# Optimization experiments

Hardware: AMD Instinct MI355X
Metric: run time of the kernel (lower is better)

The kernel has to match this reference:

```python
import jax, jax.numpy as jnp
from jax import lax
import numpy as np

B, S = 128, 512
TARGET_SIZE = 32
T = TARGET_SIZE + 4  # tag_size, START = T-2, END = T-1


def setup_inputs() -> dict:
    key = jax.random.key(0)
    k1, k2, k3, k4 = jax.random.split(key, 4)
    feats = jax.random.normal(k1, (B, S, T), dtype=jnp.float32)
    # contiguous-prefix mask (lengths in [S//2, S])
    lengths = jax.random.randint(k2, (B,), S // 2, S + 1)
    mask = (jnp.arange(S)[None, :] < lengths[:, None]).astype(jnp.int32)
    tags = jax.random.randint(k3, (B, S), 0, TARGET_SIZE).astype(jnp.int32)
    # learned transitions, with the hard constraints from __init__
    transitions = 0.1 * jax.random.normal(k4, (T, T), dtype=jnp.float32)
    transitions = transitions.at[:, T - 2].set(-1000.0)  # nothing -> START
    transitions = transitions.at[T - 1, :].set(-1000.0)  # END -> nothing
    return {"feats": feats, "transitions": transitions, "mask": mask, "tags": tags}


def _nll(feats, transitions, mask, tags):
    # feats: (B,S,T), transitions: (T,T) with [i,j] = score(prev=i -> cur=j)
    b, s, t = feats.shape
    START, END = t - 2, t - 1
    fdtype = feats.dtype

    feats_t = jnp.swapaxes(feats, 0, 1)   # (S,B,T)
    mask_t = jnp.swapaxes(mask, 0, 1)     # (S,B)

    # ---- forward algorithm (partition function) ----
    # scores[t,b,i,j] = feats[b,t,j] + transitions[i,j]
    part0 = feats_t[0] + transitions[START][None, :]  # (B,T): alpha after step 0

    def step(part, xs):
        f_step, m_step = xs  # (B,T), (B,)
        # cur[b,i,j] = feats[b,j] + trans[i,j] + part[b,i]
        cur = f_step[:, None, :] + transitions[None, :, :] + part[:, :, None]
        new_part = jax.nn.logsumexp(cur, axis=1)  # (B,T)
        part = jnp.where(m_step[:, None].astype(bool), new_part, part)
        return part, None

    part, _ = lax.scan(step, part0, (feats_t[1:], mask_t[1:]))
    final = jax.nn.logsumexp(part[:, :, None] + transitions[None, :, :], axis=1)  # (B,T)
    forward_score = jnp.sum(final[:, END])

    # ---- gold score ----
    tags_i = tags.astype(jnp.int32)
    prev_tags = jnp.concatenate(
        [jnp.full((b, 1), START, dtype=jnp.int32), tags_i[:, :-1]], axis=1)  # (B,S)
    emit = jnp.take_along_axis(feats, tags_i[:, :, None], axis=2)[:, :, 0]    # (B,S)
    trans_sc = transitions[prev_tags, tags_i]                                  # (B,S)
    tg_energy = jnp.sum((emit + trans_sc) * mask.astype(fdtype))
    lengths = jnp.sum(mask, axis=1).astype(jnp.int32)                          # (B,)
    end_ids = jnp.take_along_axis(tags_i, (lengths - 1)[:, None], axis=1)[:, 0]
    end_energy = jnp.sum(transitions[end_ids, END])
    gold_score = tg_energy + end_energy

    # average_batch = True
    return (forward_score - gold_score) / jnp.asarray(b, fdtype)


def reference(feats, transitions, mask, tags):
    return _nll(feats, transitions, mask, tags)
```

## Files before the change

### kernel.cpp

```cpp
#include <hip/hip_runtime.h>
#include <hip/hip_bf16.h>


namespace {
constexpr int kB = 128;
constexpr int kS = 512;
constexpr int kT = 36;
constexpr int kStart = 34;
constexpr int kEnd = 35;
constexpr int kP = 32;
constexpr int kL = 16;
constexpr int kEStr = 64;

typedef __bf16 bf16x4 __attribute__((ext_vector_type(4)));
typedef short short4v __attribute__((ext_vector_type(4)));
typedef float f32x4 __attribute__((ext_vector_type(4)));
typedef int int2v __attribute__((ext_vector_type(2)));

__device__ __forceinline__ float readlane_f(float v, int lane) {
    return __builtin_bit_cast(float, __builtin_amdgcn_readlane(__builtin_bit_cast(int, v), lane));
}

__device__ __forceinline__ float wave_sum(float v) {
#pragma unroll
    for (int off = 32; off; off >>= 1) v += __shfl_xor(v, off, 64);
    return v;
}

__device__ __forceinline__ int wave_sum_i(int v) {
#pragma unroll
    for (int off = 32; off; off >>= 1) v += __shfl_xor(v, off, 64);
    return v;
}

#define MF16(a, b, c) __builtin_amdgcn_mfma_f32_16x16x16bf16_1k((a), (b), (c), 0, 0, 0)


__global__ __attribute__((amdgpu_flat_work_group_size(64, 64),
                          amdgpu_waves_per_eu(2, 4)))
void crf_chunk_kernel(const float* __restrict__ feats,
                      const float* __restrict__ trans,
                      const int* __restrict__ mask,
                      __bf16* __restrict__ Hws,
                      float* __restrict__ lscws) {
    const int b = blockIdx.x;
    const int p = blockIdx.y;
    const int tid = threadIdx.x;
    const int ln = tid & 15;
    const int quad = tid >> 4;

    __shared__ __align__(16) float Etab[kL * kEStr];

    const int* mb = mask + b * kS;
    int len = 0;
#pragma unroll
    for (int k = 0; k < kS / 64; ++k) len += mb[k * 64 + tid];
    len = wave_sum_i(len);

    __bf16* Hout = Hws + (size_t)(b * kP + p) * (kT * kT);
    const int cs = (p == 0) ? 1 : p * kL;
    const int ce = min((p + 1) * kL, len);
    const int nsteps = ce - cs;

    if (nsteps <= 0) {
        for (int idx = tid; idx < kT * kT; idx += 64)
            Hout[idx] = (__bf16)((idx / kT == idx % kT) ? 1.f : 0.f);
        if (tid == 0) lscws[b * kP + p] = 0.f;
        return;
    }

    const float* fb = feats + ((size_t)b * kS + cs) * kT;
    {
        float stage[kL];
#pragma unroll
        for (int it = 0; it < kL; ++it)
            stage[it] = (tid < kT) ? fb[it * kT + tid] : 0.f;
#pragma unroll
        for (int it = 0; it < kL; ++it)
            Etab[it * kEStr + tid] = (tid < kT) ? __expf(stage[it]) : 1.0f;
    }
    __builtin_amdgcn_s_waitcnt(0);

    auto afrag = [&](int rt, int kc) {
        bf16x4 r;
        const int m = rt * 16 + ln;
#pragma unroll
        for (int e = 0; e < 4; ++e) {
            const int k = kc * 16 + quad * 4 + e;
            float v = 0.f;
            if (m < kT && k < kT) v = __expf(trans[k * kT + m]);
            r[e] = (__bf16)v;
        }
        return __builtin_bit_cast(short4v, r);
    };
    const short4v a00 = afrag(0, 0), a01 = afrag(0, 1), a02 = afrag(0, 2);
    const short4v a10 = afrag(1, 0), a11 = afrag(1, 1), a12 = afrag(1, 2);
    const short4v a20 = afrag(2, 0), a21 = afrag(2, 1), a22 = afrag(2, 2);

    auto binit = [&](int kc, int ct) {
        bf16x4 r;
        const int n = ct * 16 + ln;
#pragma unroll
        for (int e = 0; e < 4; ++e) {
            const int k = kc * 16 + quad * 4 + e;
            r[e] = (__bf16)((k == n && k < kT) ? 1.f : 0.f);
        }
        return __builtin_bit_cast(short4v, r);
    };
    short4v b00 = binit(0, 0), b01 = binit(0, 1), b02 = binit(0, 2);
    short4v b10 = binit(1, 0), b11 = binit(1, 1), b12 = binit(1, 2);
    short4v b20 = binit(2, 0), b21 = binit(2, 1), b22 = binit(2, 2);

    float logC = 0.f;
    const f32x4 z = {0.f, 0.f, 0.f, 0.f};
    for (int tl = 0; tl < nsteps; ++tl) {
        const int w11 = __builtin_amdgcn_readlane(__builtin_bit_cast(int2v, b00).x, 1);
        const float* et = &Etab[tl * kEStr + quad * 4];
        const f32x4 e0 = *(const f32x4*)(et + 0);
        const f32x4 e1 = *(const f32x4*)(et + 16);
        const f32x4 e2 = *(const f32x4*)(et + 32);

        f32x4 c00 = MF16(a00, b00, z); f32x4 c01 = MF16(a00, b01, z); f32x4 c02 = MF16(a00, b02, z);
        c00 = MF16(a01, b10, c00);     c01 = MF16(a01, b11, c01);     c02 = MF16(a01, b12, c02);
        c00 = MF16(a02, b20, c00);     c01 = MF16(a02, b21, c01);     c02 = MF16(a02, b22, c02);
        f32x4 c10 = MF16(a10, b00, z); f32x4 c11 = MF16(a10, b01, z); f32x4 c12 = MF16(a10, b02, z);
        c10 = MF16(a11, b10, c10);     c11 = MF16(a11, b11, c11);     c12 = MF16(a11, b12, c12);
        c10 = MF16(a12, b20, c10);     c11 = MF16(a12, b21, c11);     c12 = MF16(a12, b22, c12);
        f32x4 c20 = MF16(a20, b00, z); f32x4 c21 = MF16(a20, b01, z); f32x4 c22 = MF16(a20, b02, z);
        c20 = MF16(a21, b10, c20);     c21 = MF16(a21, b11, c21);     c22 = MF16(a21, b12, c22);
        c20 = MF16(a22, b20, c20);     c21 = MF16(a22, b21, c21);     c22 = MF16(a22, b22, c22);

        float rs = 1.f;
        if ((tl & 3) == 3) {
            const float s = __builtin_bit_cast(float, (unsigned)w11 & 0xFFFF0000u);
            rs = __builtin_amdgcn_rcpf(s);
            logC += __logf(s);
        }
        const f32x4 s0 = e0 * rs, s1 = e1 * rs, s2 = e2 * rs;

#define PK(cv, sv) ({ const f32x4 t_ = (cv) * (sv); bf16x4 h_;                  \
        h_[0] = (__bf16)t_[0]; h_[1] = (__bf16)t_[1];                           \
        h_[2] = (__bf16)t_[2]; h_[3] = (__bf16)t_[3];                           \
        __builtin_bit_cast(short4v, h_); })
        b00 = PK(c00, s0); b01 = PK(c01, s0); b02 = PK(c02, s0);
        b10 = PK(c10, s1); b11 = PK(c11, s1); b12 = PK(c12, s1);
        b20 = PK(c20, s2); b21 = PK(c21, s2); b22 = PK(c22, s2);
#undef PK
    }

#define STOREB(Bv, kc, ct) {                                                    \
    const bf16x4 h_ = __builtin_bit_cast(bf16x4, Bv);                           \
    const int n_ = (ct)*16 + ln;                                                \
    _Pragma("unroll") for (int e = 0; e < 4; ++e) {                             \
        const int m_ = (kc)*16 + quad * 4 + e;                                  \
        if (m_ < kT && n_ < kT) Hout[m_ * kT + n_] = h_[e]; } }
    STOREB(b00, 0, 0) STOREB(b01, 0, 1) STOREB(b02, 0, 2)
    STOREB(b10, 1, 0) STOREB(b11, 1, 1) STOREB(b12, 1, 2)
    STOREB(b20, 2, 0) STOREB(b21, 2, 1) STOREB(b22, 2, 2)
#undef STOREB
    if (tid == 0) lscws[b * kP + p] = logC;
}


#define FORK36(X) \
    X(0,0,0,0) X(1,1,0,1) X(2,2,0,2) X(3,3,0,3) \
    X(4,0,1,0) X(5,1,1,1) X(6,2,1,2) X(7,3,1,3) \
    X(8,0,2,0) X(9,1,2,1) X(10,2,2,2) X(11,3,2,3) \
    X(12,0,3,0) X(13,1,3,1) X(14,2,3,2) X(15,3,3,3) \
    X(16,0,4,0) X(17,1,4,1) X(18,2,4,2) X(19,3,4,3) \
    X(20,0,5,0) X(21,1,5,1) X(22,2,5,2) X(23,3,5,3) \
    X(24,0,6,0) X(25,1,6,1) X(26,2,6,2) X(27,3,6,3) \
    X(28,0,7,0) X(29,1,7,1) X(30,2,7,2) X(31,3,7,3) \
    X(32,0,8,0) X(33,1,8,1) X(34,2,8,2) X(35,3,8,3)

__global__ __attribute__((amdgpu_flat_work_group_size(64, 64),
                          amdgpu_waves_per_eu(1, 1)))
void crf_combine_kernel(const float* __restrict__ feats,
                        const float* __restrict__ trans,
                        const int* __restrict__ mask,
                        const int* __restrict__ tags,
                        const __bf16* __restrict__ Hws,
                        const float* __restrict__ lscws,
                        float* __restrict__ out) {
    const int b = blockIdx.x;
    const int j = threadIdx.x;
    const float* fbase = feats + (size_t)b * kS * kT;
    const int* mb = mask + b * kS;
    const int* tb = tags + b * kS;

    int len = 0;
#pragma unroll
    for (int k = 0; k < kS / 64; ++k) len += mb[k * 64 + j];
    len = wave_sum_i(len);

    const float ME = (j < kT) ? __expf(trans[j * kT + kEnd]) : 0.f;

    float a0 = -1e30f;
    if (j < kT) a0 = fbase[j] + trans[kStart * kT + j];
    float C = readlane_f(a0, 0);
    float q = __expf(a0 - C);

    const int jr = (j < kT) ? j : 0;
#pragma unroll 4
    for (int p = 0; p < kP; ++p) {
        const __bf16* rp = Hws + ((size_t)(b * kP + p) * kT + jr) * kT;
        const bf16x4 h0 = *(const bf16x4*)(rp + 0);
        const bf16x4 h1 = *(const bf16x4*)(rp + 4);
        const bf16x4 h2 = *(const bf16x4*)(rp + 8);
        const bf16x4 h3 = *(const bf16x4*)(rp + 12);
        const bf16x4 h4 = *(const bf16x4*)(rp + 16);
        const bf16x4 h5 = *(const bf16x4*)(rp + 20);
        const bf16x4 h6 = *(const bf16x4*)(rp + 24);
        const bf16x4 h7 = *(const bf16x4*)(rp + 28);
        const bf16x4 h8 = *(const bf16x4*)(rp + 32);
#define BRD2(n, a, g, c) const float bb##n = readlane_f(q, n);
        FORK36(BRD2)
#undef BRD2
        float v0 = 0.f, v1 = 0.f, v2 = 0.f, v3 = 0.f;
#define FMA2(n, a, g, c) v##a = fmaf(bb##n, (float)h##g[c], v##a);
        FORK36(FMA2)
#undef FMA2
        const float qn = (v0 + v1) + (v2 + v3);
        q = (j < kT) ? qn : 0.f;
        C += lscws[b * kP + p];
        const float s = readlane_f(q, 0);
        q *= __builtin_amdgcn_rcpf(s);
        C += __logf(s);
    }

    const float ssum = wave_sum(q * ME);
    const float forward_b = C + __logf(ssum);

    float g = 0.f;
    for (int k = j; k < kS; k += 64) {
        if (k < len) {
            const int tg = tb[k];
            const int pv = (k == 0) ? kStart : tb[k - 1];
            g += fbase[(size_t)k * kT + tg] + trans[pv * kT + tg];
        }
    }
    g = wave_sum(g);

    if (j == 0) {
        g += trans[tb[len - 1] * kT + kEnd];
        atomicAdd(out, (forward_b - g) * (1.0f / kB));
    }
}

}

extern "C" void kernel_launch(void* const* d_in, const int* in_sizes, int n_in,
                              void* d_out, int out_size, void* d_ws, size_t ws_size,
                              hipStream_t stream) {
    const float* feats = (const float*)d_in[0];
    const float* trans = (const float*)d_in[1];
    const int* mask = (const int*)d_in[2];
    const int* tags = (const int*)d_in[3];
    float* out = (float*)d_out;

    __bf16* Hws = (__bf16*)d_ws;
    float* lscws = (float*)(Hws + (size_t)kB * kP * kT * kT);

    (void)hipMemsetAsync(out, 0, sizeof(float), stream);
    crf_chunk_kernel<<<dim3(kB, kP), dim3(64), 0, stream>>>(feats, trans, mask, Hws, lscws);
    crf_combine_kernel<<<dim3(kB), dim3(64), 0, stream>>>(feats, trans, mask, tags,
                                                          Hws, lscws, out);
}
```

Baseline: 109.6 us.

## Add tree-merge stage of chunk transfer matrices and pack four chunks per block

Adds an intermediate merge kernel that multiplies groups of eight chunk transfer matrices together with MFMA, so the final serial combine walks four matrices per sequence instead of thirty-two. The chunk kernel now runs four waves per block, each handling one chunk with its own shared-memory exp table. This shortens the serial dependency chain in the final kernel at the cost of an extra kernel launch, an extra workspace round trip, and more bf16 rounding from the additional matrix products.

```diff
diff --git a/kernel.cpp b/kernel.cpp
--- a/kernel.cpp
+++ b/kernel.cpp
@@ -10,7 +10,8 @@
 constexpr int kEnd = 35;
 constexpr int kP = 32;
 constexpr int kL = 16;
-constexpr int kEStr = 64;
+constexpr int kG = 4;
+constexpr int kEStr = 48;
 
 typedef __bf16 bf16x4 __attribute__((ext_vector_type(4)));
 typedef short short4v __attribute__((ext_vector_type(4)));
@@ -35,37 +36,54 @@
 
 #define MF16(a, b, c) __builtin_amdgcn_mfma_f32_16x16x16bf16_1k((a), (b), (c), 0, 0, 0)
 
-
-__global__ __attribute__((amdgpu_flat_work_group_size(64, 64),
-                          amdgpu_waves_per_eu(2, 4)))
+#define MM27()                                                                               \
+    f32x4 c00 = MF16(a00, b00, z); f32x4 c01 = MF16(a00, b01, z); f32x4 c02 = MF16(a00, b02, z); \
+    c00 = MF16(a01, b10, c00);     c01 = MF16(a01, b11, c01);     c02 = MF16(a01, b12, c02);     \
+    c00 = MF16(a02, b20, c00);     c01 = MF16(a02, b21, c01);     c02 = MF16(a02, b22, c02);     \
+    f32x4 c10 = MF16(a10, b00, z); f32x4 c11 = MF16(a10, b01, z); f32x4 c12 = MF16(a10, b02, z); \
+    c10 = MF16(a11, b10, c10);     c11 = MF16(a11, b11, c11);     c12 = MF16(a11, b12, c12);     \
+    c10 = MF16(a12, b20, c10);     c11 = MF16(a12, b21, c11);     c12 = MF16(a12, b22, c12);     \
+    f32x4 c20 = MF16(a20, b00, z); f32x4 c21 = MF16(a20, b01, z); f32x4 c22 = MF16(a20, b02, z); \
+    c20 = MF16(a21, b10, c20);     c21 = MF16(a21, b11, c21);     c22 = MF16(a21, b12, c22);     \
+    c20 = MF16(a22, b20, c20);     c21 = MF16(a22, b21, c21);     c22 = MF16(a22, b22, c22);
+
+#define PK(cv, sv) ({ const f32x4 t_ = (cv) * (sv); bf16x4 h_;                  \
+        h_[0] = (__bf16)t_[0]; h_[1] = (__bf16)t_[1];                           \
+        h_[2] = (__bf16)t_[2]; h_[3] = (__bf16)t_[3];                           \
+        __builtin_bit_cast(short4v, h_); })
+
+
+__global__ __attribute__((amdgpu_flat_work_group_size(256, 256),
+                          amdgpu_waves_per_eu(4, 8)))
 void crf_chunk_kernel(const float* __restrict__ feats,
                       const float* __restrict__ trans,
                       const int* __restrict__ mask,
-                      __bf16* __restrict__ Hws,
-                      float* __restrict__ lscws) {
+                      __bf16* __restrict__ Hc,
+                      float* __restrict__ lsc) {
     const int b = blockIdx.x;
-    const int p = blockIdx.y;
-    const int tid = threadIdx.x;
-    const int ln = tid & 15;
-    const int quad = tid >> 4;
-
-    __shared__ __align__(16) float Etab[kL * kEStr];
+    const int wid = threadIdx.x >> 6;
+    const int lane = threadIdx.x & 63;
+    const int p = blockIdx.y * 4 + wid;
+    const int ln = lane & 15;
+    const int quad = lane >> 4;
+
+    __shared__ __align__(16) float Etab[4][kL * kEStr];
 
     const int* mb = mask + b * kS;
     int len = 0;
 #pragma unroll
-    for (int k = 0; k < kS / 64; ++k) len += mb[k * 64 + tid];
+    for (int k = 0; k < kS / 64; ++k) len += mb[k * 64 + lane];
     len = wave_sum_i(len);
 
-    __bf16* Hout = Hws + (size_t)(b * kP + p) * (kT * kT);
+    __bf16* Hout = Hc + (size_t)(b * kP + p) * (kT * kT);
     const int cs = (p == 0) ? 1 : p * kL;
     const int ce = min((p + 1) * kL, len);
     const int nsteps = ce - cs;
 
     if (nsteps <= 0) {
-        for (int idx = tid; idx < kT * kT; idx += 64)
+        for (int idx = lane; idx < kT * kT; idx += 64)
             Hout[idx] = (__bf16)((idx / kT == idx % kT) ? 1.f : 0.f);
-        if (tid == 0) lscws[b * kP + p] = 0.f;
+        if (lane == 0) lsc[b * kP + p] = 0.f;
         return;
     }
 
@@ -74,10 +92,11 @@
         float stage[kL];
 #pragma unroll
         for (int it = 0; it < kL; ++it)
-            stage[it] = (tid < kT) ? fb[it * kT + tid] : 0.f;
+            stage[it] = (lane < kT) ? fb[it * kT + lane] : 0.f;
 #pragma unroll
         for (int it = 0; it < kL; ++it)
-            Etab[it * kEStr + tid] = (tid < kT) ? __expf(stage[it]) : 1.0f;
+            if (lane < kEStr)
+                Etab[wid][it * kEStr + lane] = (lane < kT) ? __expf(stage[it]) : 1.0f;
     }
     __builtin_amdgcn_s_waitcnt(0);
 
@@ -115,20 +134,12 @@
     const f32x4 z = {0.f, 0.f, 0.f, 0.f};
     for (int tl = 0; tl < nsteps; ++tl) {
         const int w11 = __builtin_amdgcn_readlane(__builtin_bit_cast(int2v, b00).x, 1);
-        const float* et = &Etab[tl * kEStr + quad * 4];
+        const float* et = &Etab[wid][tl * kEStr + quad * 4];
         const f32x4 e0 = *(const f32x4*)(et + 0);
         const f32x4 e1 = *(const f32x4*)(et + 16);
         const f32x4 e2 = *(const f32x4*)(et + 32);
 
-        f32x4 c00 = MF16(a00, b00, z); f32x4 c01 = MF16(a00, b01, z); f32x4 c02 = MF16(a00, b02, z);
-        c00 = MF16(a01, b10, c00);     c01 = MF16(a01, b11, c01);     c02 = MF16(a01, b12, c02);
-        c00 = MF16(a02, b20, c00);     c01 = MF16(a02, b21, c01);     c02 = MF16(a02, b22, c02);
-        f32x4 c10 = MF16(a10, b00, z); f32x4 c11 = MF16(a10, b01, z); f32x4 c12 = MF16(a10, b02, z);
-        c10 = MF16(a11, b10, c10);     c11 = MF16(a11, b11, c11);     c12 = MF16(a11, b12, c12);
-        c10 = MF16(a12, b20, c10);     c11 = MF16(a12, b21, c11);     c12 = MF16(a12, b22, c12);
-        f32x4 c20 = MF16(a20, b00, z); f32x4 c21 = MF16(a20, b01, z); f32x4 c22 = MF16(a20, b02, z);
-        c20 = MF16(a21, b10, c20);     c21 = MF16(a21, b11, c21);     c22 = MF16(a21, b12, c22);
-        c20 = MF16(a22, b20, c20);     c21 = MF16(a22, b21, c21);     c22 = MF16(a22, b22, c22);
+        MM27()
 
         float rs = 1.f;
         if ((tl & 3) == 3) {
@@ -137,15 +148,9 @@
             logC += __logf(s);
         }
         const f32x4 s0 = e0 * rs, s1 = e1 * rs, s2 = e2 * rs;
-
-#define PK(cv, sv) ({ const f32x4 t_ = (cv) * (sv); bf16x4 h_;                  \
-        h_[0] = (__bf16)t_[0]; h_[1] = (__bf16)t_[1];                           \
-        h_[2] = (__bf16)t_[2]; h_[3] = (__bf16)t_[3];                           \
-        __builtin_bit_cast(short4v, h_); })
         b00 = PK(c00, s0); b01 = PK(c01, s0); b02 = PK(c02, s0);
         b10 = PK(c10, s1); b11 = PK(c11, s1); b12 = PK(c12, s1);
         b20 = PK(c20, s2); b21 = PK(c21, s2); b22 = PK(c22, s2);
-#undef PK
     }
 
 #define STOREB(Bv, kc, ct) {                                                    \
@@ -157,8 +162,88 @@
     STOREB(b00, 0, 0) STOREB(b01, 0, 1) STOREB(b02, 0, 2)
     STOREB(b10, 1, 0) STOREB(b11, 1, 1) STOREB(b12, 1, 2)
     STOREB(b20, 2, 0) STOREB(b21, 2, 1) STOREB(b22, 2, 2)
-#undef STOREB
-    if (tid == 0) lscws[b * kP + p] = logC;
+    if (lane == 0) lsc[b * kP + p] = logC;
+}
+
+
+__global__ __attribute__((amdgpu_flat_work_group_size(64, 64),
+                          amdgpu_waves_per_eu(1, 4)))
+void crf_merge_kernel(const __bf16* __restrict__ Hc,
+                      const float* __restrict__ lsc,
+                      __bf16* __restrict__ Hm,
+                      float* __restrict__ mlsc) {
+    const int b = blockIdx.x;
+    const int g = blockIdx.y;
+    const int lane = threadIdx.x;
+    const int ln = lane & 15;
+    const int quad = lane >> 4;
+    const int base = b * kP + g * 8;
+
+    float logm = 0.f;
+#pragma unroll
+    for (int i = 0; i < 8; ++i) logm += lsc[base + i];
+
+    const __bf16* H0 = Hc + (size_t)base * (kT * kT);
+    auto loadB0 = [&](int kc, int ct) {
+        bf16x4 r;
+        const int n = ct * 16 + ln;
+#pragma unroll
+        for (int e = 0; e < 4; ++e) {
+            const int k = kc * 16 + quad * 4 + e;
+            float v = 0.f;
+            if (k < kT && n < kT) v = (float)H0[k * kT + n];
+            r[e] = (__bf16)v;
+        }
+        return __builtin_bit_cast(short4v, r);
+    };
+    short4v b00 = loadB0(0, 0), b01 = loadB0(0, 1), b02 = loadB0(0, 2);
+    short4v b10 = loadB0(1, 0), b11 = loadB0(1, 1), b12 = loadB0(1, 2);
+    short4v b20 = loadB0(2, 0), b21 = loadB0(2, 1), b22 = loadB0(2, 2);
+
+    const f32x4 z = {0.f, 0.f, 0.f, 0.f};
+    for (int i = 1; i < 8; ++i) {
+        const __bf16* Hn = Hc + (size_t)(base + i) * (kT * kT);
+        auto loadA = [&](int rt, int kc) {
+            bf16x4 r;
+            const int m = rt * 16 + ln;
+            const int k0 = kc * 16 + quad * 4;
+            if (m < kT && k0 + 3 < kT) {
+                r = *(const bf16x4*)&Hn[m * kT + k0];
+            } else {
+#pragma unroll
+                for (int e = 0; e < 4; ++e)
+                    r[e] = (__bf16)((m < kT && k0 + e < kT) ? (float)Hn[m * kT + k0 + e] : 0.f);
+            }
+            return __builtin_bit_cast(short4v, r);
+        };
+        const short4v a00 = loadA(0, 0), a01 = loadA(0, 1), a02 = loadA(0, 2);
+        const short4v a10 = loadA(1, 0), a11 = loadA(1, 1), a12 = loadA(1, 2);
+        const short4v a20 = loadA(2, 0), a21 = loadA(2, 1), a22 = loadA(2, 2);
+
+        const int w11 = __builtin_amdgcn_readlane(__builtin_bit_cast(int2v, b00).x, 1);
+
+        MM27()
+
+        const float s = __builtin_bit_cast(float, (unsigned)w11 & 0xFFFF0000u);
+        const float rsf = __builtin_amdgcn_rcpf(s);
+        logm += __logf(s);
+        const f32x4 rv = {rsf, rsf, rsf, rsf};
+        b00 = PK(c00, rv); b01 = PK(c01, rv); b02 = PK(c02, rv);
+        b10 = PK(c10, rv); b11 = PK(c11, rv); b12 = PK(c12, rv);
+        b20 = PK(c20, rv); b21 = PK(c21, rv); b22 = PK(c22, rv);
+    }
+
+    __bf16* Ho = Hm + (size_t)(b * kG + g) * (kT * kT);
+#define STOREM(Bv, kc, ct) {                                                    \
+    const bf16x4 h_ = __builtin_bit_cast(bf16x4, Bv);                           \
+    const int n_ = (ct)*16 + ln;                                                \
+    _Pragma("unroll") for (int e = 0; e < 4; ++e) {                             \
+        const int m_ = (kc)*16 + quad * 4 + e;                                  \
+        if (m_ < kT && n_ < kT) Ho[m_ * kT + n_] = h_[e]; } }
+    STOREM(b00, 0, 0) STOREM(b01, 0, 1) STOREM(b02, 0, 2)
+    STOREM(b10, 1, 0) STOREM(b11, 1, 1) STOREM(b12, 1, 2)
+    STOREM(b20, 2, 0) STOREM(b21, 2, 1) STOREM(b22, 2, 2)
+    if (lane == 0) mlsc[b * kG + g] = logm;
 }
 
 
@@ -175,13 +260,13 @@
 
 __global__ __attribute__((amdgpu_flat_work_group_size(64, 64),
                           amdgpu_waves_per_eu(1, 1)))
-void crf_combine_kernel(const float* __restrict__ feats,
-                        const float* __restrict__ trans,
-                        const int* __restrict__ mask,
-                        const int* __restrict__ tags,
-                        const __bf16* __restrict__ Hws,
-                        const float* __restrict__ lscws,
-                        float* __restrict__ out) {
+void crf_final_kernel(const float* __restrict__ feats,
+                      const float* __restrict__ trans,
+                      const int* __restrict__ mask,
+                      const int* __restrict__ tags,
+                      const __bf16* __restrict__ Hm,
+                      const float* __restrict__ mlsc,
+                      float* __restrict__ out) {
     const int b = blockIdx.x;
     const int j = threadIdx.x;
     const float* fbase = feats + (size_t)b * kS * kT;
@@ -201,9 +286,9 @@
     float q = __expf(a0 - C);
 
     const int jr = (j < kT) ? j : 0;
-#pragma unroll 4
-    for (int p = 0; p < kP; ++p) {
-        const __bf16* rp = Hws + ((size_t)(b * kP + p) * kT + jr) * kT;
+#pragma unroll
+    for (int g = 0; g < kG; ++g) {
+        const __bf16* rp = Hm + ((size_t)(b * kG + g) * kT + jr) * kT;
         const bf16x4 h0 = *(const bf16x4*)(rp + 0);
         const bf16x4 h1 = *(const bf16x4*)(rp + 4);
         const bf16x4 h2 = *(const bf16x4*)(rp + 8);
@@ -213,16 +298,16 @@
         const bf16x4 h6 = *(const bf16x4*)(rp + 24);
         const bf16x4 h7 = *(const bf16x4*)(rp + 28);
         const bf16x4 h8 = *(const bf16x4*)(rp + 32);
-#define BRD2(n, a, g, c) const float bb##n = readlane_f(q, n);
+#define BRD2(n, a, g2, c) const float bb##n = readlane_f(q, n);
         FORK36(BRD2)
 #undef BRD2
         float v0 = 0.f, v1 = 0.f, v2 = 0.f, v3 = 0.f;
-#define FMA2(n, a, g, c) v##a = fmaf(bb##n, (float)h##g[c], v##a);
+#define FMA2(n, a, g2, c) v##a = fmaf(bb##n, (float)h##g2[c], v##a);
         FORK36(FMA2)
 #undef FMA2
         const float qn = (v0 + v1) + (v2 + v3);
         q = (j < kT) ? qn : 0.f;
-        C += lscws[b * kP + p];
+        C += mlsc[b * kG + g];
         const float s = readlane_f(q, 0);
         q *= __builtin_amdgcn_rcpf(s);
         C += __logf(s);
@@ -231,19 +316,19 @@
     const float ssum = wave_sum(q * ME);
     const float forward_b = C + __logf(ssum);
 
-    float g = 0.f;
+    float g2 = 0.f;
     for (int k = j; k < kS; k += 64) {
         if (k < len) {
             const int tg = tb[k];
             const int pv = (k == 0) ? kStart : tb[k - 1];
-            g += fbase[(size_t)k * kT + tg] + trans[pv * kT + tg];
-        }
-    }
-    g = wave_sum(g);
+            g2 += fbase[(size_t)k * kT + tg] + trans[pv * kT + tg];
+        }
+    }
+    g2 = wave_sum(g2);
 
     if (j == 0) {
-        g += trans[tb[len - 1] * kT + kEnd];
-        atomicAdd(out, (forward_b - g) * (1.0f / kB));
+        g2 += trans[tb[len - 1] * kT + kEnd];
+        atomicAdd(out, (forward_b - g2) * (1.0f / kB));
     }
 }
 
@@ -258,11 +343,14 @@
     const int* tags = (const int*)d_in[3];
     float* out = (float*)d_out;
 
-    __bf16* Hws = (__bf16*)d_ws;
-    float* lscws = (float*)(Hws + (size_t)kB * kP * kT * kT);
+    __bf16* Hc = (__bf16*)d_ws;
+    float* lsc = (float*)(Hc + (size_t)kB * kP * kT * kT);
+    __bf16* Hm = (__bf16*)(lsc + kB * kP);
+    float* mlsc = (float*)(Hm + (size_t)kB * kG * kT * kT);
 
     (void)hipMemsetAsync(out, 0, sizeof(float), stream);
-    crf_chunk_kernel<<<dim3(kB, kP), dim3(64), 0, stream>>>(feats, trans, mask, Hws, lscws);
-    crf_combine_kernel<<<dim3(kB), dim3(64), 0, stream>>>(feats, trans, mask, tags,
-                                                          Hws, lscws, out);
-}
+    crf_chunk_kernel<<<dim3(kB, kP / 4), dim3(256), 0, stream>>>(feats, trans, mask, Hc, lsc);
+    crf_merge_kernel<<<dim3(kB, kG), dim3(64), 0, stream>>>(Hc, lsc, Hm, mlsc);
+    crf_final_kernel<<<dim3(kB), dim3(64), 0, stream>>>(feats, trans, mask, tags,
+                                                        Hm, mlsc, out);
+}
```

Result: no change. 110.3 us (+0.7%).

## Process two chunks per block with interleaved MFMA chains and pre-multiply pairs

Applied to the files above, without the earlier changes.

Each chunk block now computes two adjacent 16-step transfer-matrix products at once, interleaving their independent MFMA chains to hide MFMA latency. It then multiplies the two products together in-block through an LDS transpose. This halves the number of matrices the serial combine kernel must fold per batch (16 instead of 32) and halves the grid size. The cost is higher register pressure, an extra 36x36 matmul per block, and fewer blocks for occupancy.

```diff
diff --git a/kernel.cpp b/kernel.cpp
--- a/kernel.cpp
+++ b/kernel.cpp
@@ -8,9 +8,10 @@
 constexpr int kT = 36;
 constexpr int kStart = 34;
 constexpr int kEnd = 35;
-constexpr int kP = 32;
 constexpr int kL = 16;
-constexpr int kEStr = 64;
+constexpr int kG = 16;
+constexpr int kEStr = 48;
+constexpr int kTS = 52;
 
 typedef __bf16 bf16x4 __attribute__((ext_vector_type(4)));
 typedef short short4v __attribute__((ext_vector_type(4)));
@@ -35,49 +36,72 @@
 
 #define MF16(a, b, c) __builtin_amdgcn_mfma_f32_16x16x16bf16_1k((a), (b), (c), 0, 0, 0)
 
+#define MM27(AP, BP, CP) \
+    f32x4 CP##_00 = MF16(AP##_00, BP##_00, z), CP##_01 = MF16(AP##_00, BP##_01, z), CP##_02 = MF16(AP##_00, BP##_02, z); \
+    f32x4 CP##_10 = MF16(AP##_10, BP##_00, z), CP##_11 = MF16(AP##_10, BP##_01, z), CP##_12 = MF16(AP##_10, BP##_02, z); \
+    f32x4 CP##_20 = MF16(AP##_20, BP##_00, z), CP##_21 = MF16(AP##_20, BP##_01, z), CP##_22 = MF16(AP##_20, BP##_02, z); \
+    CP##_00 = MF16(AP##_01, BP##_10, CP##_00); CP##_01 = MF16(AP##_01, BP##_11, CP##_01); CP##_02 = MF16(AP##_01, BP##_12, CP##_02); \
+    CP##_10 = MF16(AP##_11, BP##_10, CP##_10); CP##_11 = MF16(AP##_11, BP##_11, CP##_11); CP##_12 = MF16(AP##_11, BP##_12, CP##_12); \
+    CP##_20 = MF16(AP##_21, BP##_10, CP##_20); CP##_21 = MF16(AP##_21, BP##_11, CP##_21); CP##_22 = MF16(AP##_21, BP##_12, CP##_22); \
+    CP##_00 = MF16(AP##_02, BP##_20, CP##_00); CP##_01 = MF16(AP##_02, BP##_21, CP##_01); CP##_02 = MF16(AP##_02, BP##_22, CP##_02); \
+    CP##_10 = MF16(AP##_12, BP##_20, CP##_10); CP##_11 = MF16(AP##_12, BP##_21, CP##_11); CP##_12 = MF16(AP##_12, BP##_22, CP##_12); \
+    CP##_20 = MF16(AP##_22, BP##_20, CP##_20); CP##_21 = MF16(AP##_22, BP##_21, CP##_21); CP##_22 = MF16(AP##_22, BP##_22, CP##_22);
+
+#define PK(cv, sv) ({ const f32x4 t_ = (cv) * (sv); bf16x4 h_;                  \
+        h_[0] = (__bf16)t_[0]; h_[1] = (__bf16)t_[1];                           \
+        h_[2] = (__bf16)t_[2]; h_[3] = (__bf16)t_[3];                           \
+        __builtin_bit_cast(short4v, h_); })
+
 
 __global__ __attribute__((amdgpu_flat_work_group_size(64, 64),
                           amdgpu_waves_per_eu(2, 4)))
-void crf_chunk_kernel(const float* __restrict__ feats,
-                      const float* __restrict__ trans,
-                      const int* __restrict__ mask,
-                      __bf16* __restrict__ Hws,
-                      float* __restrict__ lscws) {
+void crf_pair_kernel(const float* __restrict__ feats,
+                     const float* __restrict__ trans,
+                     const int* __restrict__ mask,
+                     __bf16* __restrict__ Hp,
+                     float* __restrict__ lsc) {
     const int b = blockIdx.x;
-    const int p = blockIdx.y;
-    const int tid = threadIdx.x;
-    const int ln = tid & 15;
-    const int quad = tid >> 4;
-
-    __shared__ __align__(16) float Etab[kL * kEStr];
+    const int g = blockIdx.y;
+    const int lane = threadIdx.x;
+    const int ln = lane & 15;
+    const int quad = lane >> 4;
+
+    __shared__ __align__(16) float Etab[2 * kL * kEStr];
+    __shared__ __align__(16) unsigned short Tr[48 * kTS];
 
     const int* mb = mask + b * kS;
     int len = 0;
 #pragma unroll
-    for (int k = 0; k < kS / 64; ++k) len += mb[k * 64 + tid];
+    for (int k = 0; k < kS / 64; ++k) len += mb[k * 64 + lane];
     len = wave_sum_i(len);
 
-    __bf16* Hout = Hws + (size_t)(b * kP + p) * (kT * kT);
-    const int cs = (p == 0) ? 1 : p * kL;
-    const int ce = min((p + 1) * kL, len);
-    const int nsteps = ce - cs;
-
-    if (nsteps <= 0) {
-        for (int idx = tid; idx < kT * kT; idx += 64)
+    __bf16* Hout = Hp + (size_t)(b * kG + g) * (kT * kT);
+    const int p0 = 2 * g, p1 = 2 * g + 1;
+    const int cs0 = (p0 == 0) ? 1 : p0 * kL;
+    const int n0 = min((p0 + 1) * kL, len) - cs0;
+    const int cs1 = p1 * kL;
+    const int n1 = min((p1 + 1) * kL, len) - cs1;
+
+    if (n0 <= 0) {
+        for (int idx = lane; idx < kT * kT; idx += 64)
             Hout[idx] = (__bf16)((idx / kT == idx % kT) ? 1.f : 0.f);
-        if (tid == 0) lscws[b * kP + p] = 0.f;
+        if (lane == 0) lsc[b * kG + g] = 0.f;
         return;
     }
 
-    const float* fb = feats + ((size_t)b * kS + cs) * kT;
+    const float* fb = feats + (size_t)b * kS * kT;
     {
-        float stage[kL];
+        float st[2 * kL];
 #pragma unroll
         for (int it = 0; it < kL; ++it)
-            stage[it] = (tid < kT) ? fb[it * kT + tid] : 0.f;
+            st[it] = (lane < kT) ? fb[(size_t)(cs0 + it) * kT + lane] : 0.f;
 #pragma unroll
         for (int it = 0; it < kL; ++it)
-            Etab[it * kEStr + tid] = (tid < kT) ? __expf(stage[it]) : 1.0f;
+            st[kL + it] = (lane < kT) ? fb[(size_t)(cs1 + it) * kT + lane] : 0.f;
+#pragma unroll
+        for (int it = 0; it < 2 * kL; ++it)
+            if (lane < kEStr)
+                Etab[it * kEStr + lane] = (lane < kT) ? __expf(st[it]) : 1.0f;
     }
     __builtin_amdgcn_s_waitcnt(0);
 
@@ -93,9 +117,9 @@
         }
         return __builtin_bit_cast(short4v, r);
     };
-    const short4v a00 = afrag(0, 0), a01 = afrag(0, 1), a02 = afrag(0, 2);
-    const short4v a10 = afrag(1, 0), a11 = afrag(1, 1), a12 = afrag(1, 2);
-    const short4v a20 = afrag(2, 0), a21 = afrag(2, 1), a22 = afrag(2, 2);
+    const short4v a_00 = afrag(0, 0), a_01 = afrag(0, 1), a_02 = afrag(0, 2);
+    const short4v a_10 = afrag(1, 0), a_11 = afrag(1, 1), a_12 = afrag(1, 2);
+    const short4v a_20 = afrag(2, 0), a_21 = afrag(2, 1), a_22 = afrag(2, 2);
 
     auto binit = [&](int kc, int ct) {
         bf16x4 r;
@@ -107,58 +131,88 @@
         }
         return __builtin_bit_cast(short4v, r);
     };
-    short4v b00 = binit(0, 0), b01 = binit(0, 1), b02 = binit(0, 2);
-    short4v b10 = binit(1, 0), b11 = binit(1, 1), b12 = binit(1, 2);
-    short4v b20 = binit(2, 0), b21 = binit(2, 1), b22 = binit(2, 2);
+    short4v b0_00 = binit(0, 0), b0_01 = binit(0, 1), b0_02 = binit(0, 2);
+    short4v b0_10 = binit(1, 0), b0_11 = binit(1, 1), b0_12 = binit(1, 2);
+    short4v b0_20 = binit(2, 0), b0_21 = binit(2, 1), b0_22 = binit(2, 2);
+    short4v b1_00 = binit(0, 0), b1_01 = binit(0, 1), b1_02 = binit(0, 2);
+    short4v b1_10 = binit(1, 0), b1_11 = binit(1, 1), b1_12 = binit(1, 2);
+    short4v b1_20 = binit(2, 0), b1_21 = binit(2, 1), b1_22 = binit(2, 2);
 
     float logC = 0.f;
     const f32x4 z = {0.f, 0.f, 0.f, 0.f};
-    for (int tl = 0; tl < nsteps; ++tl) {
-        const int w11 = __builtin_amdgcn_readlane(__builtin_bit_cast(int2v, b00).x, 1);
-        const float* et = &Etab[tl * kEStr + quad * 4];
-        const f32x4 e0 = *(const f32x4*)(et + 0);
-        const f32x4 e1 = *(const f32x4*)(et + 16);
-        const f32x4 e2 = *(const f32x4*)(et + 32);
-
-        f32x4 c00 = MF16(a00, b00, z); f32x4 c01 = MF16(a00, b01, z); f32x4 c02 = MF16(a00, b02, z);
-        c00 = MF16(a01, b10, c00);     c01 = MF16(a01, b11, c01);     c02 = MF16(a01, b12, c02);
-        c00 = MF16(a02, b20, c00);     c01 = MF16(a02, b21, c01);     c02 = MF16(a02, b22, c02);
-        f32x4 c10 = MF16(a10, b00, z); f32x4 c11 = MF16(a10, b01, z); f32x4 c12 = MF16(a10, b02, z);
-        c10 = MF16(a11, b10, c10);     c11 = MF16(a11, b11, c11);     c12 = MF16(a11, b12, c12);
-        c10 = MF16(a12, b20, c10);     c11 = MF16(a12, b21, c11);     c12 = MF16(a12, b22, c12);
-        f32x4 c20 = MF16(a20, b00, z); f32x4 c21 = MF16(a20, b01, z); f32x4 c22 = MF16(a20, b02, z);
-        c20 = MF16(a21, b10, c20);     c21 = MF16(a21, b11, c21);     c22 = MF16(a21, b12, c22);
-        c20 = MF16(a22, b20, c20);     c21 = MF16(a22, b21, c21);     c22 = MF16(a22, b22, c22);
-
-        float rs = 1.f;
+    const int nmax = max(n0, n1);
+    for (int tl = 0; tl < nmax; ++tl) {
+        const int w11_0 = __builtin_amdgcn_readlane(__builtin_bit_cast(int2v, b0_00).x, 1);
+        const int w11_1 = __builtin_amdgcn_readlane(__builtin_bit_cast(int2v, b1_00).x, 1);
+        const float* et0 = &Etab[tl * kEStr + quad * 4];
+        const f32x4 e0a = *(const f32x4*)(et0 + 0);
+        const f32x4 e0b = *(const f32x4*)(et0 + 16);
+        const f32x4 e0c = *(const f32x4*)(et0 + 32);
+        const float* et1 = &Etab[(kL + tl) * kEStr + quad * 4];
+        const f32x4 e1a = *(const f32x4*)(et1 + 0);
+        const f32x4 e1b = *(const f32x4*)(et1 + 16);
+        const f32x4 e1c = *(const f32x4*)(et1 + 32);
+
+        MM27(a, b0, c0)
+        MM27(a, b1, c1)
+
+        float rs0 = 1.f, rs1 = 1.f;
         if ((tl & 3) == 3) {
-            const float s = __builtin_bit_cast(float, (unsigned)w11 & 0xFFFF0000u);
-            rs = __builtin_amdgcn_rcpf(s);
-            logC += __logf(s);
-        }
-        const f32x4 s0 = e0 * rs, s1 = e1 * rs, s2 = e2 * rs;
-
-#define PK(cv, sv) ({ const f32x4 t_ = (cv) * (sv); bf16x4 h_;                  \
-        h_[0] = (__bf16)t_[0]; h_[1] = (__bf16)t_[1];                           \
-        h_[2] = (__bf16)t_[2]; h_[3] = (__bf16)t_[3];                           \
-        __builtin_bit_cast(short4v, h_); })
-        b00 = PK(c00, s0); b01 = PK(c01, s0); b02 = PK(c02, s0);
-        b10 = PK(c10, s1); b11 = PK(c11, s1); b12 = PK(c12, s1);
-        b20 = PK(c20, s2); b21 = PK(c21, s2); b22 = PK(c22, s2);
-#undef PK
-    }
-
-#define STOREB(Bv, kc, ct) {                                                    \
-    const bf16x4 h_ = __builtin_bit_cast(bf16x4, Bv);                           \
+            if (tl < n0) {
+                const float s = __builtin_bit_cast(float, (unsigned)w11_0 & 0xFFFF0000u);
+                rs0 = __builtin_amdgcn_rcpf(s);
+                logC += __logf(s);
+            }
+            if (tl < n1) {
+                const float s = __builtin_bit_cast(float, (unsigned)w11_1 & 0xFFFF0000u);
+                rs1 = __builtin_amdgcn_rcpf(s);
+                logC += __logf(s);
+            }
+        }
+        const f32x4 s0a = e0a * rs0, s0b = e0b * rs0, s0c = e0c * rs0;
+        const f32x4 s1a = e1a * rs1, s1b = e1b * rs1, s1c = e1c * rs1;
+
+        if (tl < n0) {
+            b0_00 = PK(c0_00, s0a); b0_01 = PK(c0_01, s0a); b0_02 = PK(c0_02, s0a);
+            b0_10 = PK(c0_10, s0b); b0_11 = PK(c0_11, s0b); b0_12 = PK(c0_12, s0b);
+            b0_20 = PK(c0_20, s0c); b0_21 = PK(c0_21, s0c); b0_22 = PK(c0_22, s0c);
+        }
+        if (tl < n1) {
+            b1_00 = PK(c1_00, s1a); b1_01 = PK(c1_01, s1a); b1_02 = PK(c1_02, s1a);
+            b1_10 = PK(c1_10, s1b); b1_11 = PK(c1_11, s1b); b1_12 = PK(c1_12, s1b);
+            b1_20 = PK(c1_20, s1c); b1_21 = PK(c1_21, s1c); b1_22 = PK(c1_22, s1c);
+        }
+    }
+
+#define TW(Bv, kc, ct) *(short4v*)&Tr[((ct)*16 + ln) * kTS + (kc)*16 + quad * 4] = Bv;
+    TW(b1_00, 0, 0) TW(b1_01, 0, 1) TW(b1_02, 0, 2)
+    TW(b1_10, 1, 0) TW(b1_11, 1, 1) TW(b1_12, 1, 2)
+    TW(b1_20, 2, 0) TW(b1_21, 2, 1) TW(b1_22, 2, 2)
+#undef TW
+    __builtin_amdgcn_s_waitcnt(0);
+#define TR(rt, kc) (*(const short4v*)&Tr[((rt)*16 + ln) * kTS + (kc)*16 + quad * 4])
+    const short4v pa_00 = TR(0, 0), pa_01 = TR(0, 1), pa_02 = TR(0, 2);
+    const short4v pa_10 = TR(1, 0), pa_11 = TR(1, 1), pa_12 = TR(1, 2);
+    const short4v pa_20 = TR(2, 0), pa_21 = TR(2, 1), pa_22 = TR(2, 2);
+#undef TR
+
+    MM27(pa, b0, cp)
+
+    const float sP = readlane_f(cp_00[1], 1);
+    const float rsP = __builtin_amdgcn_rcpf(sP);
+    logC += __logf(sP);
+    const f32x4 rv = {rsP, rsP, rsP, rsP};
+#define STOREC(cv, rt, ct) {                                                    \
+    const bf16x4 h_ = __builtin_bit_cast(bf16x4, PK(cv, rv));                   \
     const int n_ = (ct)*16 + ln;                                                \
     _Pragma("unroll") for (int e = 0; e < 4; ++e) {                             \
-        const int m_ = (kc)*16 + quad * 4 + e;                                  \
+        const int m_ = (rt)*16 + quad * 4 + e;                                  \
         if (m_ < kT && n_ < kT) Hout[m_ * kT + n_] = h_[e]; } }
-    STOREB(b00, 0, 0) STOREB(b01, 0, 1) STOREB(b02, 0, 2)
-    STOREB(b10, 1, 0) STOREB(b11, 1, 1) STOREB(b12, 1, 2)
-    STOREB(b20, 2, 0) STOREB(b21, 2, 1) STOREB(b22, 2, 2)
-#undef STOREB
-    if (tid == 0) lscws[b * kP + p] = logC;
+    STOREC(cp_00, 0, 0) STOREC(cp_01, 0, 1) STOREC(cp_02, 0, 2)
+    STOREC(cp_10, 1, 0) STOREC(cp_11, 1, 1) STOREC(cp_12, 1, 2)
+    STOREC(cp_20, 2, 0) STOREC(cp_21, 2, 1) STOREC(cp_22, 2, 2)
+#undef STOREC
+    if (lane == 0) lsc[b * kG + g] = logC;
 }
 
 
@@ -175,13 +229,13 @@
 
 __global__ __attribute__((amdgpu_flat_work_group_size(64, 64),
                           amdgpu_waves_per_eu(1, 1)))
-void crf_combine_kernel(const float* __restrict__ feats,
-                        const float* __restrict__ trans,
-                        const int* __restrict__ mask,
-                        const int* __restrict__ tags,
-                        const __bf16* __restrict__ Hws,
-                        const float* __restrict__ lscws,
-                        float* __restrict__ out) {
+void crf_final_kernel(const float* __restrict__ feats,
+                      const float* __restrict__ trans,
+                      const int* __restrict__ mask,
+                      const int* __restrict__ tags,
+                      const __bf16* __restrict__ Hp,
+                      const float* __restrict__ lsc,
+                      float* __restrict__ out) {
     const int b = blockIdx.x;
     const int j = threadIdx.x;
     const float* fbase = feats + (size_t)b * kS * kT;
@@ -201,9 +255,8 @@
     float q = __expf(a0 - C);
 
     const int jr = (j < kT) ? j : 0;
-#pragma unroll 4
-    for (int p = 0; p < kP; ++p) {
-        const __bf16* rp = Hws + ((size_t)(b * kP + p) * kT + jr) * kT;
+    for (int g = 0; g < kG; ++g) {
+        const __bf16* rp = Hp + ((size_t)(b * kG + g) * kT + jr) * kT;
         const bf16x4 h0 = *(const bf16x4*)(rp + 0);
         const bf16x4 h1 = *(const bf16x4*)(rp + 4);
         const bf16x4 h2 = *(const bf16x4*)(rp + 8);
@@ -213,16 +266,16 @@
         const bf16x4 h6 = *(const bf16x4*)(rp + 24);
         const bf16x4 h7 = *(const bf16x4*)(rp + 28);
         const bf16x4 h8 = *(const bf16x4*)(rp + 32);
-#define BRD2(n, a, g, c) const float bb##n = readlane_f(q, n);
+#define BRD2(n, a, g2, c) const float bb##n = readlane_f(q, n);
         FORK36(BRD2)
 #undef BRD2
         float v0 = 0.f, v1 = 0.f, v2 = 0.f, v3 = 0.f;
-#define FMA2(n, a, g, c) v##a = fmaf(bb##n, (float)h##g[c], v##a);
+#define FMA2(n, a, g2, c) v##a = fmaf(bb##n, (float)h##g2[c], v##a);
         FORK36(FMA2)
 #undef FMA2
         const float qn = (v0 + v1) + (v2 + v3);
         q = (j < kT) ? qn : 0.f;
-        C += lscws[b * kP + p];
+        C += lsc[b * kG + g];
         const float s = readlane_f(q, 0);
         q *= __builtin_amdgcn_rcpf(s);
         C += __logf(s);
@@ -231,19 +284,19 @@
     const float ssum = wave_sum(q * ME);
     const float forward_b = C + __logf(ssum);
 
-    float g = 0.f;
+    float g2 = 0.f;
     for (int k = j; k < kS; k += 64) {
         if (k < len) {
             const int tg = tb[k];
             const int pv = (k == 0) ? kStart : tb[k - 1];
-            g += fbase[(size_t)k * kT + tg] + trans[pv * kT + tg];
-        }
-    }
-    g = wave_sum(g);
+            g2 += fbase[(size_t)k * kT + tg] + trans[pv * kT + tg];
+        }
+    }
+    g2 = wave_sum(g2);
 
     if (j == 0) {
-        g += trans[tb[len - 1] * kT + kEnd];
-        atomicAdd(out, (forward_b - g) * (1.0f / kB));
+        g2 += trans[tb[len - 1] * kT + kEnd];
+        atomicAdd(out, (forward_b - g2) * (1.0f / kB));
     }
 }
 
@@ -258,11 +311,11 @@
     const int* tags = (const int*)d_in[3];
     float* out = (float*)d_out;
 
-    __bf16* Hws = (__bf16*)d_ws;
-    float* lscws = (float*)(Hws + (size_t)kB * kP * kT * kT);
+    __bf16* Hp = (__bf16*)d_ws;
+    float* lsc = (float*)(Hp + (size_t)kB * kG * kT * kT);
 
     (void)hipMemsetAsync(out, 0, sizeof(float), stream);
-    crf_chunk_kernel<<<dim3(kB, kP), dim3(64), 0, stream>>>(feats, trans, mask, Hws, lscws);
-    crf_combine_kernel<<<dim3(kB), dim3(64), 0, stream>>>(feats, trans, mask, tags,
-                                                          Hws, lscws, out);
-}
+    crf_pair_kernel<<<dim3(kB, kG), dim3(64), 0, stream>>>(feats, trans, mask, Hp, lsc);
+    crf_final_kernel<<<dim3(kB), dim3(64), 0, stream>>>(feats, trans, mask, tags,
+                                                        Hp, lsc, out);
+}
```

New measurement: 114.4 us. 4.4% more time.
